# Optimization experiments

Hardware: AMD Instinct MI355X
Metric: run time of the kernel (lower is better)

## Reference

```python
import jax, jax.numpy as jnp
import numpy as np
import math

B, S, D, H, M, R = 4, 1024, 1024, 16, 4, 64
DH = D // H
EPS = 1e-8

def setup_inputs() -> dict:
    key = jax.random.key(0)
    ks = jax.random.split(key, 8)
    sc = 0.02
    return {
        'x': jax.random.normal(ks[0], (B, S, D), jnp.float32),
        'Wk': jax.random.normal(ks[1], (D, D), jnp.float32) * sc,
        'bk': jnp.zeros((D,), jnp.float32),
        'Wq': jax.random.normal(ks[2], (D, D), jnp.float32) * sc,
        'bq': jnp.zeros((D,), jnp.float32),
        'Wv': jax.random.normal(ks[3], (D, D), jnp.float32) * sc,
        'bv': jnp.zeros((D,), jnp.float32),
        'mask1': jax.random.normal(ks[4], (M, R, S), jnp.float32) * sc,
        'mask2': jax.random.normal(ks[5], (M, R, S), jnp.float32) * sc,
        'roll_back': jax.random.randint(ks[6], (M, S, S), 0, S, jnp.int64),
    }

def reference(x, Wk, bk, Wq, bq, Wv, bv, mask1, mask2, roll_back):
    def proj(W, b):
        # torch Linear: x @ W^T + b ; reshape to [B, H, S, DH]
        y = jnp.dot(x, W.T) + b
        return y.reshape(B, S, H, DH).transpose(0, 2, 1, 3)
    k = proj(Wk, bk)
    q = proj(Wq, bq)
    v = proj(Wv, bv)
    # learnable low-rank mask: [M, S, S]
    learnable_mask = jnp.einsum('mrs,mrt->mst', mask1, mask2)
    # gather along last dim with roll_back indices
    gathered = jnp.take_along_axis(learnable_mask, roll_back, axis=-1)  # [M, S, S]
    att = jnp.einsum('bhsd,bhtd->bhst', q, k) / math.sqrt(DH)  # [B, H, S, S]
    att = att.reshape(B, H // M, M, S, S) * gathered[None, None]
    att = att.reshape(B, H, S, S)
    # Frobenius norm over last two dims per (B, H)
    fro = jnp.sqrt(jnp.sum(att * att, axis=(-2, -1), keepdims=True))
    att = att / (fro + EPS)
    out = jnp.einsum('bhst,bhtd->bhsd', att, v)
    return out.transpose(0, 2, 1, 3).reshape(B, S, D)
```

## Files before the change

### kernel.cpp

```cpp
#include <hip/hip_runtime.h>
#include <hip/hip_bf16.h>
#include <stdint.h>

typedef __attribute__((ext_vector_type(8))) __bf16 bf16x8;
typedef __attribute__((ext_vector_type(4))) float  f32x4;
typedef __attribute__((ext_vector_type(16))) float f32x16;

__device__ __forceinline__ ushort f2bf(float f) {
    union { float f; uint32_t u; } v; v.f = f;
    uint32_t u = v.u;
    uint32_t r = 0x7FFFu + ((u >> 16) & 1u);
    return (ushort)((u + r) >> 16);
}
__device__ __forceinline__ float bf2f(ushort u) {
    union { uint32_t u; float f; } v; v.u = ((uint32_t)u) << 16;
    return v.f;
}

typedef __attribute__((address_space(3))) uint32_t lds_u32_t;
typedef const __attribute__((address_space(1))) uint32_t glb_u32_t;
__device__ __forceinline__ void async_copy16(const void* g, void* l) {
    __builtin_amdgcn_global_load_lds((glb_u32_t*)g, (lds_u32_t*)l, 16, 0, 0);
}

__global__ __launch_bounds__(256) void convert_all(
    const float* __restrict__ x, const float* __restrict__ wk,
    const float* __restrict__ wq, const float* __restrict__ wv,
    ushort* __restrict__ xb, ushort* __restrict__ wball)
{
    int i = blockIdx.x * 256 + threadIdx.x;
    const float* src; ushort* dst; int j;
    if (i < 1048576) { src = x; dst = xb; j = i; }
    else {
        int t = i - 1048576;
        int z = t >> 18;
        j = t & 262143;
        src = (z == 0) ? wk : (z == 1) ? wq : wv;
        dst = wball + z * 1048576;
    }
    float4 f = ((const float4*)src)[j];
    ushort4 o;
    o.x = f2bf(f.x); o.y = f2bf(f.y); o.z = f2bf(f.z); o.w = f2bf(f.w);
    ((ushort4*)dst)[j] = o;
}

__global__ __launch_bounds__(256) void proj_gemm(
    const ushort* __restrict__ xb, const ushort* __restrict__ wball,
    const float* __restrict__ bk, const float* __restrict__ bq, const float* __restrict__ bv,
    ushort* __restrict__ kd, ushort* __restrict__ qd, ushort* __restrict__ vd)
{
    __shared__ ushort As[128 * 64];
    __shared__ ushort Bs[128 * 64];
    const int z = blockIdx.z;
    const int row0 = blockIdx.x * 128;
    const int col0 = blockIdx.y * 128;
    const ushort* wb = wball + z * 1048576;
    const int tid = threadIdx.x;
    const int lane = tid & 63, wave = tid >> 6;
    const int quad = lane >> 4, m15 = lane & 15;
    const int wr = wave >> 1, wc = wave & 1;

    f32x4 acc[4][4];
    for (int i = 0; i < 4; i++)
        for (int j = 0; j < 4; j++) acc[i][j] = (f32x4){0.f, 0.f, 0.f, 0.f};

    for (int kk = 0; kk < 1024; kk += 64) {
        __syncthreads();
        #pragma unroll
        for (int i = 0; i < 4; i++) {
            int c = tid + i * 256;
            int r = c >> 3, cjp = c & 7;
            int cj = cjp ^ (r & 7);
            async_copy16(&xb[(row0 + r) * 1024 + kk + cj * 8], &As[c * 8]);
            async_copy16(&wb[(col0 + r) * 1024 + kk + cj * 8], &Bs[c * 8]);
        }
        __syncthreads();
        #pragma unroll
        for (int kh = 0; kh < 2; kh++) {
            bf16x8 af[4], bfv[4];
            #pragma unroll
            for (int fr = 0; fr < 4; fr++) {
                int row = wr * 64 + fr * 16 + m15;
                int q4 = kh * 4 + quad;
                af[fr] = *(const bf16x8*)&As[row * 64 + ((q4 ^ (row & 7)) * 8)];
            }
            #pragma unroll
            for (int fc = 0; fc < 4; fc++) {
                int row = wc * 64 + fc * 16 + m15;
                int q4 = kh * 4 + quad;
                bfv[fc] = *(const bf16x8*)&Bs[row * 64 + ((q4 ^ (row & 7)) * 8)];
            }
            #pragma unroll
            for (int fr = 0; fr < 4; fr++)
                #pragma unroll
                for (int fc = 0; fc < 4; fc++)
                    acc[fr][fc] = __builtin_amdgcn_mfma_f32_16x16x32_bf16(af[fr], bfv[fc], acc[fr][fc], 0, 0, 0);
        }
    }

    const float* bias = (z == 0) ? bk : (z == 1) ? bq : bv;
    ushort* dstA = (z == 0) ? kd : qd;
    for (int fr = 0; fr < 4; fr++) {
        int ibase = row0 + wr * 64 + fr * 16 + quad * 4;
        int b_ = ibase >> 10, s = ibase & 1023;
        for (int fc = 0; fc < 4; fc++) {
            int j = col0 + wc * 64 + fc * 16 + m15;
            int h = j >> 6, dh = j & 63;
            float bb = bias[j];
            if (z < 2) {
                for (int r = 0; r < 4; r++)
                    dstA[((b_ * 16 + h) * 1024 + (s + r)) * 64 + dh] = f2bf(acc[fr][fc][r] + bb);
            } else {
                ushort4 o;
                o.x = f2bf(acc[fr][fc][0] + bb);
                o.y = f2bf(acc[fr][fc][1] + bb);
                o.z = f2bf(acc[fr][fc][2] + bb);
                o.w = f2bf(acc[fr][fc][3] + bb);
                *(ushort4*)&vd[((b_ * 16 + h) * 64 + dh) * 1024 + s] = o;
            }
        }
    }
}

__global__ __launch_bounds__(256) void mask_fused(
    const float* __restrict__ m1, const float* __restrict__ m2,
    const int* __restrict__ rb, ushort* __restrict__ gth)
{
    __shared__ float As8[64 * 8];
    __shared__ float lmS[8 * 1024];
    const int s0 = blockIdx.x * 8;
    const int m = blockIdx.y;
    const int tid = threadIdx.x;

    if (tid < 128) {
        int r = tid >> 1, half = tid & 1;
        *(float4*)&As8[r * 8 + half * 4] =
            *(const float4*)&m1[(m * 64 + r) * 1024 + s0 + half * 4];
    }
    __syncthreads();

    f32x4 acc8[8];
    #pragma unroll
    for (int s = 0; s < 8; s++) acc8[s] = (f32x4){0.f, 0.f, 0.f, 0.f};
    const float* m2b = m2 + m * 65536 + tid * 4;
    #pragma unroll 4
    for (int r = 0; r < 64; r++) {
        float4 b4 = *(const float4*)&m2b[r * 1024];
        f32x4 b = (f32x4){b4.x, b4.y, b4.z, b4.w};
        #pragma unroll
        for (int s = 0; s < 8; s++) {
            float a = As8[r * 8 + s];
            acc8[s] += a * b;
        }
    }
    #pragma unroll
    for (int s = 0; s < 8; s++)
        *(f32x4*)&lmS[s * 1024 + tid * 4] = acc8[s];
    __syncthreads();

    const int base = (m * 1024 + s0) * 1024;
    #pragma unroll
    for (int i = 0; i < 8; i++) {
        int c = tid + i * 256;
        int row = c >> 8, j = (c & 255) * 4;
        int4 idx = *(const int4*)&rb[base + row * 1024 + j];
        ushort4 o;
        o.x = f2bf(lmS[row * 1024 + (idx.x & 1023)] * 0.125f);
        o.y = f2bf(lmS[row * 1024 + (idx.y & 1023)] * 0.125f);
        o.z = f2bf(lmS[row * 1024 + (idx.z & 1023)] * 0.125f);
        o.w = f2bf(lmS[row * 1024 + (idx.w & 1023)] * 0.125f);
        *(ushort4*)&gth[base + row * 1024 + j] = o;
    }
}

__global__ __launch_bounds__(256, 2) void attention(
    const ushort* __restrict__ qd, const ushort* __restrict__ kd, const ushort* __restrict__ vd,
    const ushort* __restrict__ gth, float* __restrict__ O, float* __restrict__ ss)
{
    __shared__ ushort Ks[64 * 72];
    __shared__ ushort Vs[64 * 72];
    __shared__ ushort Ps[64 * 72];
    __shared__ ushort Ms[64 * 72];
    __shared__ float red[4];
    const int s0 = blockIdx.x * 64;
    const int bh = blockIdx.y;
    const int mm = bh & 3;
    const int tid = threadIdx.x, lane = tid & 63, wave = tid >> 6;
    const int l31 = lane & 31, hl = lane >> 5;
    const int wr2 = wave >> 1, wc2 = wave & 1;

    #pragma unroll
    for (int i = 0; i < 2; i++) {
        int c = tid + i * 256;
        int r = c >> 3, off = (c & 7) * 8;
        *(uint4*)&Ms[r * 72 + off] = *(const uint4*)&qd[(bh * 1024 + s0 + r) * 64 + off];
    }
    __syncthreads();
    bf16x8 qf[4];
    #pragma unroll
    for (int kk = 0; kk < 4; kk++)
        qf[kk] = *(const bf16x8*)&Ms[(wr2 * 32 + l31) * 72 + kk * 16 + hl * 8];

    f32x16 oacc;
    #pragma unroll
    for (int i = 0; i < 16; i++) oacc[i] = 0.f;
    float ssacc = 0.f;
    const ushort* gbase = gth + mm * 1048576 + s0 * 1024;

    for (int t0 = 0; t0 < 1024; t0 += 64) {
        __syncthreads();
        #pragma unroll
        for (int i = 0; i < 2; i++) {
            int c = tid + i * 256;
            int r = c >> 3, off = (c & 7) * 8;
            *(uint4*)&Ks[r * 72 + off] = *(const uint4*)&kd[(bh * 1024 + t0 + r) * 64 + off];
            *(uint4*)&Vs[r * 72 + off] = *(const uint4*)&vd[(bh * 64 + r) * 1024 + t0 + off];
            *(uint4*)&Ms[r * 72 + off] = *(const uint4*)&gbase[r * 1024 + t0 + off];
        }
        __syncthreads();

        f32x16 p;
        #pragma unroll
        for (int i = 0; i < 16; i++) p[i] = 0.f;
        #pragma unroll
        for (int kk = 0; kk < 4; kk++) {
            bf16x8 b = *(const bf16x8*)&Ks[(wc2 * 32 + l31) * 72 + kk * 16 + hl * 8];
            p = __builtin_amdgcn_mfma_f32_32x32x16_bf16(qf[kk], b, p, 0, 0, 0);
        }
        {
            const int col = wc2 * 32 + l31;
            #pragma unroll
            for (int reg = 0; reg < 16; reg++) {
                int row = wr2 * 32 + (reg & 3) + 8 * (reg >> 2) + 4 * hl;
                float pv = p[reg] * bf2f(Ms[row * 72 + col]);
                ssacc += pv * pv;
                Ps[row * 72 + col] = f2bf(pv);
            }
        }
        __syncthreads();
        #pragma unroll
        for (int kk = 0; kk < 4; kk++) {
            bf16x8 a = *(const bf16x8*)&Ps[(wr2 * 32 + l31) * 72 + kk * 16 + hl * 8];
            bf16x8 b = *(const bf16x8*)&Vs[(wc2 * 32 + l31) * 72 + kk * 16 + hl * 8];
            oacc = __builtin_amdgcn_mfma_f32_32x32x16_bf16(a, b, oacc, 0, 0, 0);
        }
    }
    #pragma unroll
    for (int reg = 0; reg < 16; reg++) {
        int s = s0 + wr2 * 32 + (reg & 3) + 8 * (reg >> 2) + 4 * hl;
        int dh = wc2 * 32 + l31;
        O[(bh * 1024 + s) * 64 + dh] = oacc[reg];
    }
    for (int off = 32; off; off >>= 1) ssacc += __shfl_down(ssacc, off, 64);
    if (lane == 0) red[wave] = ssacc;
    __syncthreads();
    if (tid == 0) atomicAdd(&ss[bh], red[0] + red[1] + red[2] + red[3]);
}

__global__ __launch_bounds__(256) void normalize_out(const float* __restrict__ O,
                                                     const float* __restrict__ ss,
                                                     float* __restrict__ out)
{
    int gid = blockIdx.x * 256 + threadIdx.x;
    int e = gid * 4;
    int bh = e >> 16;
    float inv = 1.f / (sqrtf(ss[bh]) + 1e-8f);
    float4 v4 = *(const float4*)&O[e];
    int b_ = bh >> 4, h = bh & 15;
    int s = (e >> 6) & 1023, dh = e & 63;
    float4 o4 = {v4.x * inv, v4.y * inv, v4.z * inv, v4.w * inv};
    *(float4*)&out[((b_ * 1024 + s) * 16 + h) * 64 + dh] = o4;
}

extern "C" void kernel_launch(void* const* d_in, const int* in_sizes, int n_in,
                              void* d_out, int out_size, void* d_ws, size_t ws_size,
                              hipStream_t stream) {
    const float* x  = (const float*)d_in[0];
    const float* Wk = (const float*)d_in[1];
    const float* bk = (const float*)d_in[2];
    const float* Wq = (const float*)d_in[3];
    const float* bq = (const float*)d_in[4];
    const float* Wv = (const float*)d_in[5];
    const float* bv = (const float*)d_in[6];
    const float* m1 = (const float*)d_in[7];
    const float* m2 = (const float*)d_in[8];
    const int*   rb = (const int*)d_in[9];
    float* out = (float*)d_out;

    char* ws = (char*)d_ws;
    ushort* xb    = (ushort*)(ws);
    ushort* wball = (ushort*)(ws + 8388608);
    ushort* kd    = (ushort*)(ws + 14680064);
    ushort* qd    = (ushort*)(ws + 23068672);
    ushort* vd    = (ushort*)(ws + 31457280);
    float*  O     = (float*)(ws + 39845888);
    ushort* gth   = (ushort*)(ws + 56623104);
    float*  ssb   = (float*)(ws + 65011712);

    convert_all<<<7168, 256, 0, stream>>>(x, Wk, Wq, Wv, xb, wball);
    proj_gemm<<<dim3(32, 8, 3), 256, 0, stream>>>(xb, wball, bk, bq, bv, kd, qd, vd);
    mask_fused<<<dim3(128, 4), 256, 0, stream>>>(m1, m2, rb, gth);
    hipMemsetAsync(ssb, 0, 64 * sizeof(float), stream);
    attention<<<dim3(16, 64), 256, 0, stream>>>(qd, kd, vd, gth, O, ssb);
    normalize_out<<<4096, 256, 0, stream>>>(O, ssb, out);
}
```

Before: 204.4 us.

## Double-buffer projection GEMM LDS and register-prefetch attention K/V/mask tiles

```diff
diff --git a/kernel.cpp b/kernel.cpp
--- a/kernel.cpp
+++ b/kernel.cpp
@@ -44,13 +44,13 @@
     ((ushort4*)dst)[j] = o;
 }
 
-__global__ __launch_bounds__(256) void proj_gemm(
+__global__ __launch_bounds__(256, 2) void proj_gemm(
     const ushort* __restrict__ xb, const ushort* __restrict__ wball,
     const float* __restrict__ bk, const float* __restrict__ bq, const float* __restrict__ bv,
     ushort* __restrict__ kd, ushort* __restrict__ qd, ushort* __restrict__ vd)
 {
-    __shared__ ushort As[128 * 64];
-    __shared__ ushort Bs[128 * 64];
+    __shared__ ushort As[2][128 * 64];
+    __shared__ ushort Bs[2][128 * 64];
     const int z = blockIdx.z;
     const int row0 = blockIdx.x * 128;
     const int col0 = blockIdx.y * 128;
@@ -64,17 +64,23 @@
     for (int i = 0; i < 4; i++)
         for (int j = 0; j < 4; j++) acc[i][j] = (f32x4){0.f, 0.f, 0.f, 0.f};
 
-    for (int kk = 0; kk < 1024; kk += 64) {
-        __syncthreads();
+    auto stage = [&](int buf, int kk) {
         #pragma unroll
         for (int i = 0; i < 4; i++) {
             int c = tid + i * 256;
             int r = c >> 3, cjp = c & 7;
             int cj = cjp ^ (r & 7);
-            async_copy16(&xb[(row0 + r) * 1024 + kk + cj * 8], &As[c * 8]);
-            async_copy16(&wb[(col0 + r) * 1024 + kk + cj * 8], &Bs[c * 8]);
-        }
+            async_copy16(&xb[(row0 + r) * 1024 + kk + cj * 8], &As[buf][c * 8]);
+            async_copy16(&wb[(col0 + r) * 1024 + kk + cj * 8], &Bs[buf][c * 8]);
+        }
+    };
+
+    stage(0, 0);
+    for (int it = 0; it < 16; it++) {
         __syncthreads();
+        if (it < 15) stage((it + 1) & 1, (it + 1) * 64);
+        const ushort* Ab = As[it & 1];
+        const ushort* Bb = Bs[it & 1];
         #pragma unroll
         for (int kh = 0; kh < 2; kh++) {
             bf16x8 af[4], bfv[4];
@@ -82,13 +88,13 @@
             for (int fr = 0; fr < 4; fr++) {
                 int row = wr * 64 + fr * 16 + m15;
                 int q4 = kh * 4 + quad;
-                af[fr] = *(const bf16x8*)&As[row * 64 + ((q4 ^ (row & 7)) * 8)];
+                af[fr] = *(const bf16x8*)&Ab[row * 64 + ((q4 ^ (row & 7)) * 8)];
             }
             #pragma unroll
             for (int fc = 0; fc < 4; fc++) {
                 int row = wc * 64 + fc * 16 + m15;
                 int q4 = kh * 4 + quad;
-                bfv[fc] = *(const bf16x8*)&Bs[row * 64 + ((q4 ^ (row & 7)) * 8)];
+                bfv[fc] = *(const bf16x8*)&Bb[row * 64 + ((q4 ^ (row & 7)) * 8)];
             }
             #pragma unroll
             for (int fr = 0; fr < 4; fr++)
@@ -173,7 +179,7 @@
     }
 }
 
-__global__ __launch_bounds__(256, 2) void attention(
+__global__ __launch_bounds__(256, 3) void attention(
     const ushort* __restrict__ qd, const ushort* __restrict__ kd, const ushort* __restrict__ vd,
     const ushort* __restrict__ gth, float* __restrict__ O, float* __restrict__ ss)
 {
@@ -207,17 +213,38 @@
     float ssacc = 0.f;
     const ushort* gbase = gth + mm * 1048576 + s0 * 1024;
 
+    uint4 kr[2], vr[2], mr[2];
+    #pragma unroll
+    for (int i = 0; i < 2; i++) {
+        int c = tid + i * 256;
+        int r = c >> 3, off = (c & 7) * 8;
+        kr[i] = *(const uint4*)&kd[(bh * 1024 + r) * 64 + off];
+        vr[i] = *(const uint4*)&vd[(bh * 64 + r) * 1024 + off];
+        mr[i] = *(const uint4*)&gbase[r * 1024 + off];
+    }
+
     for (int t0 = 0; t0 < 1024; t0 += 64) {
         __syncthreads();
         #pragma unroll
         for (int i = 0; i < 2; i++) {
             int c = tid + i * 256;
             int r = c >> 3, off = (c & 7) * 8;
-            *(uint4*)&Ks[r * 72 + off] = *(const uint4*)&kd[(bh * 1024 + t0 + r) * 64 + off];
-            *(uint4*)&Vs[r * 72 + off] = *(const uint4*)&vd[(bh * 64 + r) * 1024 + t0 + off];
-            *(uint4*)&Ms[r * 72 + off] = *(const uint4*)&gbase[r * 1024 + t0 + off];
+            *(uint4*)&Ks[r * 72 + off] = kr[i];
+            *(uint4*)&Vs[r * 72 + off] = vr[i];
+            *(uint4*)&Ms[r * 72 + off] = mr[i];
         }
         __syncthreads();
+        if (t0 < 960) {
+            int tn = t0 + 64;
+            #pragma unroll
+            for (int i = 0; i < 2; i++) {
+                int c = tid + i * 256;
+                int r = c >> 3, off = (c & 7) * 8;
+                kr[i] = *(const uint4*)&kd[(bh * 1024 + tn + r) * 64 + off];
+                vr[i] = *(const uint4*)&vd[(bh * 64 + r) * 1024 + tn + off];
+                mr[i] = *(const uint4*)&gbase[r * 1024 + tn + off];
+            }
+        }
 
         f32x16 p;
         #pragma unroll
```

Result: slower. 275.4 us (+34.7%).
